# Kernel optimization log

Hardware: AMD Instinct MI355X
Metric: run time of the kernel (lower is better)

## Reference

```python
import jax, jax.numpy as jnp
import numpy as np

NEG = -1e9

def setup_inputs() -> dict:
    key = jax.random.key(0)
    ks = jax.random.split(key, 10)
    B, T, S, D, H = 128, 64, 64, 64, 64
    A = D + H + D  # attention mlp input dim
    inp = {
        'segmented_emb': jax.random.normal(ks[0], (B, T, S, D), jnp.float32),
        'segmented_mask': jax.random.randint(ks[1], (B, T, S), 0, 2, jnp.int32),
        'target_emb': jax.random.normal(ks[2], (B, D), jnp.float32),
        'pos_w1': jax.random.normal(ks[3], (1, H), jnp.float32) * 0.3,
        'pos_b1': jnp.zeros((H,), jnp.float32),
        'pos_w2': jax.random.normal(ks[4], (H, H), jnp.float32) * (1.0 / np.sqrt(H)),
        'pos_b2': jnp.zeros((H,), jnp.float32),
        'att_w1': jax.random.normal(ks[5], (A, H), jnp.float32) * (1.0 / np.sqrt(A)),
        'att_b1': jnp.zeros((H,), jnp.float32),
        'att_w2': jax.random.normal(ks[6], (H, 1), jnp.float32) * (1.0 / np.sqrt(H)),
        'att_b2': jnp.zeros((1,), jnp.float32),
        'proj_w': jax.random.normal(ks[7], (D, D), jnp.float32) * (1.0 / np.sqrt(D)),
        'proj_b': jnp.zeros((D,), jnp.float32),
        'ln_gamma': jnp.ones((D,), jnp.float32),
        'ln_beta': jnp.zeros((D,), jnp.float32),
    }
    return inp


def reference(segmented_emb, segmented_mask, target_emb,
              pos_w1, pos_b1, pos_w2, pos_b2,
              att_w1, att_b1, att_w2, att_b2,
              proj_w, proj_b, ln_gamma, ln_beta):
    B, T, S, D = segmented_emb.shape
    # normalized positions (S, 1)
    positions = (jnp.arange(S, dtype=jnp.float32) / max(S - 1, 1))[:, None]
    # position MLP: (S, H) -- same for every (b, t)
    pos_enc = jax.nn.relu(positions @ pos_w1 + pos_b1) @ pos_w2 + pos_b2  # (S, H)
    H = pos_enc.shape[-1]
    # attention MLP layer 1 on concat([emb, pos, target]) without materializing concat:
    # split att_w1 rows into the three blocks and sum partial projections.
    w_emb, w_pos, w_tgt = att_w1[:D], att_w1[D:D + H], att_w1[D + H:]
    h = (jnp.einsum('btsd,dh->btsh', segmented_emb, w_emb)
         + (pos_enc @ w_pos)[None, None]              # (1,1,S,H)
         + (target_emb @ w_tgt)[:, None, None]        # (B,1,1,H)
         + att_b1)
    h = jax.nn.relu(h)
    scores = (h @ att_w2)[..., 0] + att_b2[0]          # (B,T,S)
    scores = jnp.where(segmented_mask == 0, NEG, scores)
    attn = jax.nn.softmax(scores, axis=-1)             # (B,T,S)
    seg = jnp.einsum('bts,btsd->btd', attn, segmented_emb)
    seg = seg @ proj_w + proj_b                        # (B,T,D)
    mu = jnp.mean(seg, axis=-1, keepdims=True)
    var = jnp.var(seg, axis=-1, keepdims=True)
    seg = (seg - mu) / jnp.sqrt(var + 1e-5) * ln_gamma + ln_beta
    return seg
```

## Files before the change

### kernel.cpp

```cpp
#include <hip/hip_runtime.h>
#include <math.h>

#define NEG_INF -1000000000.0f

__global__ __launch_bounds__(64) void doe_pre_kernel(
    const float* __restrict__ pos_w1, const float* __restrict__ pos_b1,
    const float* __restrict__ pos_w2, const float* __restrict__ pos_b2,
    const float* __restrict__ att_w1, const float* __restrict__ att_b1,
    const float* __restrict__ target_emb,
    float* __restrict__ posc, float* __restrict__ tgtc)
{
    const int tid = threadIdx.x;
    if (blockIdx.x < 64) {
        const int s = blockIdx.x;
        __shared__ float p1[64];
        __shared__ float pe[64];
        float pos = (float)s * (1.0f / 63.0f);
        p1[tid] = fmaxf(fmaf(pos, pos_w1[tid], pos_b1[tid]), 0.0f);
        __syncthreads();
        float acc = pos_b2[tid];
        #pragma unroll
        for (int h = 0; h < 64; ++h) acc = fmaf(p1[h], pos_w2[h * 64 + tid], acc);
        pe[tid] = acc;
        __syncthreads();
        float pc = att_b1[tid];
        #pragma unroll
        for (int h = 0; h < 64; ++h) pc = fmaf(pe[h], att_w1[(64 + h) * 64 + tid], pc);
        posc[s * 64 + tid] = pc;
    } else {
        const int b = blockIdx.x - 64;
        const float* trow = target_emb + b * 64;
        float acc = 0.0f;
        #pragma unroll
        for (int d = 0; d < 64; ++d) acc = fmaf(trow[d], att_w1[(128 + d) * 64 + tid], acc);
        tgtc[b * 64 + tid] = acc;
    }
}

__device__ __forceinline__ void fma4rows(float acc[64], const float4 a,
                                         const float* __restrict__ w0)
{
    #pragma unroll
    for (int j = 0; j < 64; ++j) {
        float t0 = fmaf(a.w, w0[192 + j], acc[j]);
        t0 = fmaf(a.z, w0[128 + j], t0);
        t0 = fmaf(a.y, w0[64 + j], t0);
        acc[j] = fmaf(a.x, w0[j], t0);
    }
}

__global__ __launch_bounds__(256, 4) void doe_main_kernel(
    const float* __restrict__ seg_emb, const int* __restrict__ smask,
    const float* __restrict__ att_w1, const float* __restrict__ att_w2,
    const float* __restrict__ att_b2, const float* __restrict__ proj_w,
    const float* __restrict__ proj_b, const float* __restrict__ ln_g,
    const float* __restrict__ ln_b, const float* __restrict__ posc,
    const float* __restrict__ tgtc, float* __restrict__ out)
{
    const int w    = threadIdx.x >> 6;
    const int lane = threadIdx.x & 63;
    const int g    = (blockIdx.x << 2) | w;
    const int b    = g >> 6;
    const int s    = lane;

    const float4* rp4 = (const float4*)(seg_emb + (size_t)g * 4096 + s * 64);
    float4 c0 = rp4[0], c1 = rp4[1], c2 = rp4[2], c3 = rp4[3];

    const int mval = smask[(g << 6) | s];

    float acc[64];
    {
        const float4* pp4 = (const float4*)(posc + s * 64);
        const float*  tr  = tgtc + b * 64;
        #pragma unroll
        for (int jq = 0; jq < 16; ++jq) {
            float4 pv = pp4[jq];
            acc[4 * jq + 0] = pv.x + tr[4 * jq + 0];
            acc[4 * jq + 1] = pv.y + tr[4 * jq + 1];
            acc[4 * jq + 2] = pv.z + tr[4 * jq + 2];
            acc[4 * jq + 3] = pv.w + tr[4 * jq + 3];
        }
    }

    #pragma unroll 1
    for (int dq = 0; dq < 3; ++dq) {
        float4 n0 = rp4[4 * dq + 4], n1 = rp4[4 * dq + 5];
        float4 n2 = rp4[4 * dq + 6], n3 = rp4[4 * dq + 7];
        const float* wq = att_w1 + dq * 1024;
        fma4rows(acc, c0, wq);
        fma4rows(acc, c1, wq + 256);
        fma4rows(acc, c2, wq + 512);
        fma4rows(acc, c3, wq + 768);
        c0 = n0; c1 = n1; c2 = n2; c3 = n3;
    }
    {
        const float* wq = att_w1 + 3 * 1024;
        fma4rows(acc, c0, wq);
        fma4rows(acc, c1, wq + 256);
        fma4rows(acc, c2, wq + 512);
        fma4rows(acc, c3, wq + 768);
    }

    float sc = att_b2[0];
    #pragma unroll
    for (int j = 0; j < 64; ++j) sc = fmaf(fmaxf(acc[j], 0.0f), att_w2[j], sc);
    if (mval == 0) sc = NEG_INF;

    float mx = sc;
    #pragma unroll
    for (int off = 32; off; off >>= 1) mx = fmaxf(mx, __shfl_xor(mx, off));
    float e = __expf(sc - mx);
    float sum = e;
    #pragma unroll
    for (int off = 32; off; off >>= 1) sum += __shfl_xor(sum, off);
    const float p = e / sum;

    const float* colb = seg_emb + (size_t)g * 4096 + lane;
    float segv = 0.0f;
    #pragma unroll
    for (int s2 = 0; s2 < 64; ++s2) {
        float av = __shfl(p, s2);
        segv = fmaf(av, colb[s2 * 64], segv);
    }

    float o = proj_b[lane];
    #pragma unroll
    for (int d2 = 0; d2 < 64; ++d2) {
        float sv = __shfl(segv, d2);
        o = fmaf(sv, proj_w[d2 * 64 + lane], o);
    }

    float ssum = o;
    #pragma unroll
    for (int off = 32; off; off >>= 1) ssum += __shfl_xor(ssum, off);
    float mu = ssum * (1.0f / 64.0f);
    float df = o - mu;
    float vsum = df * df;
    #pragma unroll
    for (int off = 32; off; off >>= 1) vsum += __shfl_xor(vsum, off);
    float var = vsum * (1.0f / 64.0f);
    float inv = 1.0f / sqrtf(var + 1e-5f);
    out[(g << 6) | lane] = fmaf(df * inv, ln_g[lane], ln_b[lane]);
}

extern "C" void kernel_launch(void* const* d_in, const int* in_sizes, int n_in,
                              void* d_out, int out_size, void* d_ws, size_t ws_size,
                              hipStream_t stream)
{
    const float* seg_emb    = (const float*)d_in[0];
    const int*   smask      = (const int*)  d_in[1];
    const float* target_emb = (const float*)d_in[2];
    const float* pos_w1     = (const float*)d_in[3];
    const float* pos_b1     = (const float*)d_in[4];
    const float* pos_w2     = (const float*)d_in[5];
    const float* pos_b2     = (const float*)d_in[6];
    const float* att_w1     = (const float*)d_in[7];
    const float* att_b1     = (const float*)d_in[8];
    const float* att_w2     = (const float*)d_in[9];
    const float* att_b2     = (const float*)d_in[10];
    const float* proj_w     = (const float*)d_in[11];
    const float* proj_b     = (const float*)d_in[12];
    const float* ln_g       = (const float*)d_in[13];
    const float* ln_b       = (const float*)d_in[14];
    float* out = (float*)d_out;

    float* posc = (float*)d_ws;
    float* tgtc = posc + 4096;

    doe_pre_kernel<<<192, 64, 0, stream>>>(pos_w1, pos_b1, pos_w2, pos_b2,
                                           att_w1, att_b1, target_emb, posc, tgtc);
    doe_main_kernel<<<2048, 256, 0, stream>>>(seg_emb, smask, att_w1, att_w2,
                                              att_b2, proj_w, proj_b, ln_g, ln_b,
                                              posc, tgtc, out);
}
```

Before: 263.2 us.

## Split hidden accumulation into two 32-wide halves to raise occupancy

```diff
diff --git a/kernel.cpp b/kernel.cpp
--- a/kernel.cpp
+++ b/kernel.cpp
@@ -26,7 +26,7 @@
         float pc = att_b1[tid];
         #pragma unroll
         for (int h = 0; h < 64; ++h) pc = fmaf(pe[h], att_w1[(64 + h) * 64 + tid], pc);
-        posc[s * 64 + tid] = pc;
+        posc[(tid >> 2) * 256 + s * 4 + (tid & 3)] = pc;
     } else {
         const int b = blockIdx.x - 64;
         const float* trow = target_emb + b * 64;
@@ -37,11 +37,11 @@
     }
 }
 
-__device__ __forceinline__ void fma4rows(float acc[64], const float4 a,
-                                         const float* __restrict__ w0)
+__device__ __forceinline__ void fma4rows32(float acc[32], const float4 a,
+                                           const float* __restrict__ w0)
 {
     #pragma unroll
-    for (int j = 0; j < 64; ++j) {
+    for (int j = 0; j < 32; ++j) {
         float t0 = fmaf(a.w, w0[192 + j], acc[j]);
         t0 = fmaf(a.z, w0[128 + j], t0);
         t0 = fmaf(a.y, w0[64 + j], t0);
@@ -49,7 +49,7 @@
     }
 }
 
-__global__ __launch_bounds__(256, 4) void doe_main_kernel(
+__global__ __launch_bounds__(256, 6) void doe_main_kernel(
     const float* __restrict__ seg_emb, const int* __restrict__ smask,
     const float* __restrict__ att_w1, const float* __restrict__ att_w2,
     const float* __restrict__ att_b2, const float* __restrict__ proj_w,
@@ -64,46 +64,54 @@
     const int s    = lane;
 
     const float4* rp4 = (const float4*)(seg_emb + (size_t)g * 4096 + s * 64);
-    float4 c0 = rp4[0], c1 = rp4[1], c2 = rp4[2], c3 = rp4[3];
 
     const int mval = smask[(g << 6) | s];
 
-    float acc[64];
-    {
-        const float4* pp4 = (const float4*)(posc + s * 64);
-        const float*  tr  = tgtc + b * 64;
+    float sc = att_b2[0];
+
+    #pragma unroll 1
+    for (int h = 0; h < 2; ++h) {
+        const int jbase = h << 5;
+
+        float acc[32];
+        {
+            const float4* pq = (const float4*)posc + (h * 8) * 64 + s;
+            const float*  tr = tgtc + b * 64 + jbase;
+            #pragma unroll
+            for (int jq = 0; jq < 8; ++jq) {
+                float4 pv = pq[jq * 64];
+                acc[4 * jq + 0] = pv.x + tr[4 * jq + 0];
+                acc[4 * jq + 1] = pv.y + tr[4 * jq + 1];
+                acc[4 * jq + 2] = pv.z + tr[4 * jq + 2];
+                acc[4 * jq + 3] = pv.w + tr[4 * jq + 3];
+            }
+        }
+
+        float4 c0 = rp4[0], c1 = rp4[1], c2 = rp4[2], c3 = rp4[3];
+        #pragma unroll 1
+        for (int dq = 0; dq < 3; ++dq) {
+            float4 n0 = rp4[4 * dq + 4], n1 = rp4[4 * dq + 5];
+            float4 n2 = rp4[4 * dq + 6], n3 = rp4[4 * dq + 7];
+            const float* wq = att_w1 + dq * 1024 + jbase;
+            fma4rows32(acc, c0, wq);
+            fma4rows32(acc, c1, wq + 256);
+            fma4rows32(acc, c2, wq + 512);
+            fma4rows32(acc, c3, wq + 768);
+            c0 = n0; c1 = n1; c2 = n2; c3 = n3;
+        }
+        {
+            const float* wq = att_w1 + 3072 + jbase;
+            fma4rows32(acc, c0, wq);
+            fma4rows32(acc, c1, wq + 256);
+            fma4rows32(acc, c2, wq + 512);
+            fma4rows32(acc, c3, wq + 768);
+        }
+
+        const float* w2 = att_w2 + jbase;
         #pragma unroll
-        for (int jq = 0; jq < 16; ++jq) {
-            float4 pv = pp4[jq];
-            acc[4 * jq + 0] = pv.x + tr[4 * jq + 0];
-            acc[4 * jq + 1] = pv.y + tr[4 * jq + 1];
-            acc[4 * jq + 2] = pv.z + tr[4 * jq + 2];
-            acc[4 * jq + 3] = pv.w + tr[4 * jq + 3];
-        }
+        for (int j = 0; j < 32; ++j) sc = fmaf(fmaxf(acc[j], 0.0f), w2[j], sc);
     }
 
-    #pragma unroll 1
-    for (int dq = 0; dq < 3; ++dq) {
-        float4 n0 = rp4[4 * dq + 4], n1 = rp4[4 * dq + 5];
-        float4 n2 = rp4[4 * dq + 6], n3 = rp4[4 * dq + 7];
-        const float* wq = att_w1 + dq * 1024;
-        fma4rows(acc, c0, wq);
-        fma4rows(acc, c1, wq + 256);
-        fma4rows(acc, c2, wq + 512);
-        fma4rows(acc, c3, wq + 768);
-        c0 = n0; c1 = n1; c2 = n2; c3 = n3;
-    }
-    {
-        const float* wq = att_w1 + 3 * 1024;
-        fma4rows(acc, c0, wq);
-        fma4rows(acc, c1, wq + 256);
-        fma4rows(acc, c2, wq + 512);
-        fma4rows(acc, c3, wq + 768);
-    }
-
-    float sc = att_b2[0];
-    #pragma unroll
-    for (int j = 0; j < 64; ++j) sc = fmaf(fmaxf(acc[j], 0.0f), att_w2[j], sc);
     if (mval == 0) sc = NEG_INF;
 
     float mx = sc;
```

Measured after the change: 306.6 us. +16.5%, slower.
